# Kernel optimization log

Hardware: AMD Instinct MI355X
Metric: run time of the kernel (lower is better)

## Reference

```python
import jax, jax.numpy as jnp
import numpy as np

MC = 16384
IND_T = 96
N_MAT = 4
N_STRIKES = 21


def _init_linear(key, fan_in, fan_out, prefix=()):
    k1, k2 = jax.random.split(key)
    lim = 1.0 / np.sqrt(fan_in)
    W = jax.random.uniform(k1, prefix + (fan_in, fan_out), minval=-lim, maxval=lim, dtype=jnp.float32)
    b = jax.random.uniform(k2, prefix + (fan_out,), minval=-lim, maxval=lim, dtype=jnp.float32)
    return W, b


def setup_inputs() -> dict:
    key = jax.random.key(0)
    ks = jax.random.split(key, 14)
    z = jax.random.normal(ks[0], (MC, IND_T), dtype=jnp.float32)
    zz = jax.random.normal(ks[1], (MC, IND_T), dtype=jnp.float32)
    timegrid = jnp.arange(IND_T + 1, dtype=jnp.float32) / 365.0  # daily grid
    maturities = jnp.array([24, 48, 72, 96], dtype=jnp.int32)    # in days
    strikes = jnp.linspace(0.8, 1.2, N_STRIKES, dtype=jnp.float32)
    sv_W1, sv_b1 = _init_linear(ks[2], 3, 100)
    sv_W2, sv_b2 = _init_linear(ks[3], 100, 100)
    sv_W3, sv_b3 = _init_linear(ks[4], 100, 1)
    vh_W1, vh_b1 = _init_linear(ks[5], 2, 20, (N_MAT,))
    vh_W2, vh_b2 = _init_linear(ks[6], 20, N_STRIKES, (N_MAT,))
    vd_W1, vd_b1 = _init_linear(ks[7], 1, 20)
    vd_W2, vd_b2 = _init_linear(ks[8], 20, 1)
    vv_W1, vv_b1 = _init_linear(ks[9], 1, 20)
    vv_W2, vv_b2 = _init_linear(ks[10], 20, 1)
    v0 = jax.random.uniform(ks[11], (1,), dtype=jnp.float32) * 0.1
    rho = jnp.ones((1,), dtype=jnp.float32) * -2.0
    return dict(S0=jnp.float32(1.0), rate=jnp.float32(0.05), z=z, zz=zz,
                timegrid=timegrid, strikes=strikes, v0=v0, rho=rho,
                sv_W1=sv_W1, sv_b1=sv_b1, sv_W2=sv_W2, sv_b2=sv_b2, sv_W3=sv_W3, sv_b3=sv_b3,
                vh_W1=vh_W1, vh_b1=vh_b1, vh_W2=vh_W2, vh_b2=vh_b2,
                vd_W1=vd_W1, vd_b1=vd_b1, vd_W2=vd_W2, vd_b2=vd_b2,
                vv_W1=vv_W1, vv_b1=vv_b1, vv_W2=vv_W2, vv_b2=vv_b2,
                maturities=maturities)


def reference(S0, rate, z, zz, timegrid, strikes, v0, rho,
              sv_W1, sv_b1, sv_W2, sv_b2, sv_W3, sv_b3,
              vh_W1, vh_b1, vh_W2, vh_b2,
              vd_W1, vd_b1, vd_W2, vd_b2,
              vv_W1, vv_b1, vv_W2, vv_b2,
              maturities):
    sg = jax.lax.stop_gradient
    mc = z.shape[0]
    n_mat = vh_W1.shape[0]
    n_strikes = strikes.shape[0]

    def s_vol(x):  # [MC,3] -> [MC,1], softplus output
        h1 = jax.nn.relu(x @ sv_W1 + sv_b1)
        h2 = jax.nn.relu(h1 @ sv_W2 + sv_b2)
        return jax.nn.softplus(h2 @ sv_W3 + sv_b3)

    def v_drift(v):  # [MC,1] -> [MC,1]
        return jax.nn.relu(v @ vd_W1 + vd_b1) @ vd_W2 + vd_b2

    def v_vol(v):  # [MC,1] -> [MC,1], softplus output
        return jax.nn.softplus(jax.nn.relu(v @ vv_W1 + vv_b1) @ vv_W2 + vv_b2)

    def vanilla_hedge_all(x):  # [MC,2] -> [MC, n_strikes, n_mat] (one net per maturity)
        h1 = jax.nn.relu(jnp.einsum('mi,kio->kmo', x, vh_W1) + vh_b1[:, None, :])
        out = jax.nn.softplus(jnp.einsum('kmo,koj->kmj', h1, vh_W2) + vh_b2[:, None, :])
        return jnp.transpose(out, (1, 2, 0))

    rho_t = jnp.tanh(rho)[0]
    days = jnp.round(timegrid * 365.0).astype(jnp.int32)       # [IND_T+1]
    le = days[1:, None] <= maturities[None, :]                  # [IND_T, n_mat]
    idx_net = jnp.argmax(le, axis=1)                            # first live maturity per step
    is_mat = jnp.any(days[1:, None] == maturities[None, :], axis=1)
    mat_idx = jnp.arange(n_mat)

    Slog0 = jnp.log(jnp.full((mc, 1), S0, dtype=jnp.float32))
    V0 = jnp.full((mc, 1), 1.0, dtype=jnp.float32) * jax.nn.sigmoid(v0)[0] * 0.5
    cv0 = jnp.zeros((mc, n_strikes, n_mat), dtype=jnp.float32)
    pv0 = jnp.zeros((n_mat, n_strikes), dtype=jnp.float32)

    xs = (z.T[:, :, None], zz.T[:, :, None], timegrid[:-1], timegrid[1:], idx_net, is_mat)

    def step(carry, x):
        Slog_old, V_old, cv, pv_h, pv_var = carry
        z_i, zz_i, t0, t1, idx, im = x
        h = t1 - t0
        sqh = jnp.sqrt(h)
        dW = sqh * z_i                                          # [MC,1]
        dB = rho_t * dW + jnp.sqrt(1.0 - rho_t ** 2) * sqh * zz_i
        ones_t = jnp.full((mc, 1), 1.0, dtype=jnp.float32) * t0
        pd = s_vol(jnp.concatenate([ones_t, Slog_old, V_old], axis=1))  # price diffusion
        cv_fwd = vanilla_hedge_all(jnp.concatenate([ones_t, sg(Slog_old)], axis=1))
        V_new = V_old + v_drift(V_old) * h + v_vol(V_old) * dB
        drift = rate - 0.5 * pd ** 2
        diff = pd * dW
        drift_c = 1.0 + jnp.abs(sg(drift)) * sqh                # tamed Euler
        diff_c = 1.0 + jnp.abs(sg(pd)) * sqh
        Slog_new = Slog_old + drift * h / drift_c + diff / diff_c
        S_new = jnp.exp(Slog_new)
        S_old = jnp.exp(Slog_old)
        dS = jnp.exp(-rate * t1) * S_new - jnp.exp(-rate * t0) * S_old  # [MC,1]
        mask = (mat_idx >= idx).astype(cv.dtype)                # live maturities only
        cv = cv + mask[None, None, :] * cv_fwd * sg(dS)[:, :, None]
        # hedged vanilla (call) prices collected at maturity steps
        payoff = jnp.exp(-rate * t1) * jnp.maximum(S_new - strikes[None, :], 0.0)
        price = payoff - cv[:, :, idx]                          # [MC, n_strikes]
        pv = jnp.mean(price, axis=0)
        pvar = jnp.var(price, axis=0, ddof=1)
        sel = (mat_idx == idx)[:, None] & im
        pv_h = jnp.where(sel, pv[None, :], pv_h)
        pv_var = jnp.where(sel, pvar[None, :], pv_var)
        return (Slog_new, V_new, cv, pv_h, pv_var), None

    (_, _, _, pv_h, pv_var), _ = jax.lax.scan(step, (Slog0, V0, cv0, pv0, pv0), xs)
    return jnp.stack([pv_h, pv_var])  # [2, n_mat, n_strikes]
```

## Files before the change

kernel.cpp:

```cpp
#include <hip/hip_runtime.h>
#include <hip/hip_bf16.h>
#include <math.h>


#define MC      16384
#define NSTEP   96
#define BLOCK   1024
#define NGROUP  256
#define NPAIR   84

typedef short bf16x8 __attribute__((ext_vector_type(8)));
typedef float f32x4  __attribute__((ext_vector_type(4)));

union U8 { uint4 u; bf16x8 v; };
union BF2U { __hip_bfloat162 b; unsigned u; };

__device__ __forceinline__ unsigned bf16rne(float x) {
    unsigned u = __float_as_uint(x);
    return (u + 0x7FFFu + ((u >> 16) & 1u)) >> 16;
}
__device__ __forceinline__ unsigned pk2(float lo, float hi) {
    BF2U t; t.b = __float22bfloat162_rn(make_float2(lo, hi));
    return t.u;
}
__device__ __forceinline__ float sp(float x) {
    return fmaxf(x, 0.f) + __logf(1.f + __expf(-fabsf(x)));
}

__global__ __launch_bounds__(BLOCK, 4)
void lsv_sim(const float* __restrict__ S0p,   const float* __restrict__ ratep,
             const float* __restrict__ z,     const float* __restrict__ zzg,
             const float* __restrict__ strikesg,
             const float* __restrict__ v0p,   const float* __restrict__ rhop,
             const float* __restrict__ svW1,  const float* __restrict__ svb1,
             const float* __restrict__ svW2,  const float* __restrict__ svb2,
             const float* __restrict__ svW3,  const float* __restrict__ svb3,
             const float* __restrict__ vhW1,  const float* __restrict__ vhb1,
             const float* __restrict__ vhW2,  const float* __restrict__ vhb2,
             const float* __restrict__ vdW1,  const float* __restrict__ vdb1,
             const float* __restrict__ vdW2,  const float* __restrict__ vdb2,
             const float* __restrict__ vvW1,  const float* __restrict__ vvb1,
             const float* __restrict__ vvW2,  const float* __restrict__ vvb2,
             const int*   __restrict__ mats,
             float* __restrict__ psum, float* __restrict__ psq)
{
    __shared__ __align__(16) unsigned short H1c[16 * 64 * 8];
    __shared__ __align__(16) float W1f[16 * 32];
    __shared__ __align__(16) float WH1f[16 * 32];
    __shared__ __align__(16) float B2T[128], W3T[128];
    __shared__ float RED[64 * 4];
    __shared__ float VDl[2][64], VVl[2][64];
    __shared__ float PSs[4][32], PSq[4][32];
    __shared__ float VW[128];

    const int tid  = threadIdx.x;
    const int lane = tid & 63;
    const int w    = __builtin_amdgcn_readfirstlane(tid >> 6);
    const int quad = lane >> 4;
    const int col  = lane & 15;
    const int gpath = blockIdx.x * 64 + lane;

    const int pt = w & 3;
    const int jg = w >> 2;
    const int hm = w >> 2;

    for (int e = tid; e < 128; e += BLOCK) {
        float v = 0.f;
        if      (e < 20)             v = vdW1[e];
        else if (e < 40)             v = vdb1[e - 20];
        else if (e < 60)             v = vdW2[e - 40];
        else if (e >= 64 && e < 84)  v = vvW1[e - 64];
        else if (e >= 84 && e < 104) v = vvb1[e - 84];
        else if (e >= 104 && e < 124)v = vvW2[e - 104];
        else if (e == 124)           v = vdb2[0];
        else if (e == 125)           v = vvb2[0];
        VW[e] = v;
        B2T[e] = (e < 100) ? svb2[e] : 0.f;
        W3T[e] = (e < 100) ? svW3[e] : 0.f;
    }
    for (int e = tid; e < 512; e += BLOCK) {
        const int kc2 = e >> 5, r5 = e & 31, grp = r5 >> 3, kk = kc2 * 8 + (r5 & 7);
        float v = 0.f;
        if (kk < 100) v = (grp == 0) ? svW1[kk] : (grp == 1) ? svW1[100 + kk]
                        : (grp == 2) ? svW1[200 + kk] : svb1[kk];
        W1f[e] = v;
    }
    for (int e = tid; e < 512; e += BLOCK) {
        const int hq = e >> 5, r5 = e & 31, grp = r5 >> 3;
        const int hmm = hq >> 2, qq = hq & 3;
        const int j = qq * 8 + (r5 & 7);
        float v = 0.f;
        if (j < 20 && grp < 3)
            v = (grp == 0) ? vhW1[hmm * 40 + j] : (grp == 1) ? vhW1[hmm * 40 + 20 + j]
                                                : vhb1[hmm * 20 + j];
        WH1f[e] = v;
    }

    const float rate  = ratep[0];
    const float S0    = S0p[0];
    const float rho_t = tanhf(rhop[0]);
    const float srho  = sqrtf(1.f - rho_t * rho_t);
    const float b3    = svb3[0];
    int matr[4];
#pragma unroll
    for (int k = 0; k < 4; k++) matr[k] = mats[k];

    bf16x8 Af[4][2];
#pragma unroll
    for (int c = 0; c < 4; c++)
#pragma unroll
        for (int t = 0; t < 2; t++) {
            U8 tt;
#pragma unroll
            for (int e2 = 0; e2 < 4; e2++) {
                const int k0 = 32 * c + 8 * quad + 2 * e2;
                const int j  = (2 * jg + t) * 16 + col;
                const float v0 = (k0     < 100 && j < 100) ? svW2[k0 * 100 + j]       : 0.f;
                const float v1 = (k0 + 1 < 100 && j < 100) ? svW2[(k0 + 1) * 100 + j] : 0.f;
                (&tt.u.x)[e2] = bf16rne(v0) | (bf16rne(v1) << 16);
            }
            Af[c][t] = tt.v;
        }
    bf16x8 Ah[2];
#pragma unroll
    for (int st = 0; st < 2; st++) {
        U8 tt;
#pragma unroll
        for (int e2 = 0; e2 < 4; e2++) {
            const int j0 = 8 * quad + 2 * e2, j1 = j0 + 1;
            const int s  = st * 16 + col;
            const float v0 = (j0 < 20 && s < 21) ? vhW2[hm * 420 + j0 * 21 + s] : 0.f;
            const float v1 = (j1 < 20 && s < 21) ? vhW2[hm * 420 + j1 * 21 + s] : 0.f;
            (&tt.u.x)[e2] = bf16rne(v0) | (bf16rne(v1) << 16);
        }
        Ah[st] = tt.v;
    }
    float b2h0[4], b2h1[4], K0a[4], K1a[4];
#pragma unroll
    for (int r = 0; r < 4; r++) {
        const int s0 = quad * 4 + r, s1 = 16 + quad * 4 + r;
        b2h0[r] = vhb2[hm * 21 + s0];
        K0a[r]  = strikesg[s0];
        b2h1[r] = (s1 < 21) ? vhb2[hm * 21 + s1] : 0.f;
        K1a[r]  = (s1 < 21) ? strikesg[s1] : 1e30f;
    }

    float Slog = __logf(S0);
    float S    = __expf(Slog);
    float V    = (1.f / (1.f + __expf(-v0p[0]))) * 0.5f;
    f32x4 cv0 = {0.f, 0.f, 0.f, 0.f};
    f32x4 cv1 = {0.f, 0.f, 0.f, 0.f};
    float Slog_prev = 0.f, dS_prev = 0.f, disc1_prev = 1.f, t0_prev = 0.f;
    int   idx_prev = 0;
    bool  im_prev  = false;

    const float* zrow  = z   + (size_t)gpath * NSTEP;
    const float* zzrow = zzg + (size_t)gpath * NSTEP;

    const int path = pt * 16 + col;
    const int kc   = jg * 4 + quad;

    __syncthreads();

    auto hedge_step = [&]() {
        if (hm >= idx_prev) {
            const float slp = __shfl(Slog_prev, path);
            U8 b;
#pragma unroll
            for (int hh = 0; hh < 2; hh++) {
                const float* Wp = WH1f + (hm * 4 + quad) * 32 + hh * 4;
                const float4 wt4 = *reinterpret_cast<const float4*>(Wp);
                const float4 ws4 = *reinterpret_cast<const float4*>(Wp + 8);
                const float4 bb4 = *reinterpret_cast<const float4*>(Wp + 16);
                const float x0 = fmaxf(bb4.x + t0_prev * wt4.x + slp * ws4.x, 0.f);
                const float x1 = fmaxf(bb4.y + t0_prev * wt4.y + slp * ws4.y, 0.f);
                const float x2 = fmaxf(bb4.z + t0_prev * wt4.z + slp * ws4.z, 0.f);
                const float x3 = fmaxf(bb4.w + t0_prev * wt4.w + slp * ws4.w, 0.f);
                (&b.u.x)[2 * hh]     = pk2(x0, x1);
                (&b.u.x)[2 * hh + 1] = pk2(x2, x3);
            }
            const f32x4 z4 = {0.f, 0.f, 0.f, 0.f};
            const f32x4 D0 = __builtin_amdgcn_mfma_f32_16x16x32_bf16(Ah[0], b.v, z4, 0, 0, 0);
            const f32x4 D1 = __builtin_amdgcn_mfma_f32_16x16x32_bf16(Ah[1], b.v, z4, 0, 0, 0);
            const float dsP = __shfl(dS_prev, path);
#pragma unroll
            for (int r = 0; r < 4; r++) {
                cv0[r] += sp(D0[r] + b2h0[r]) * dsP;
                cv1[r] += sp(D1[r] + b2h1[r]) * dsP;
            }
            if (im_prev && hm == idx_prev) {
                const float Sp = __shfl(S, path);
                float p0[4], q0[4], p1[4], q1[4];
#pragma unroll
                for (int r = 0; r < 4; r++) {
                    p0[r] = disc1_prev * fmaxf(Sp - K0a[r], 0.f) - cv0[r];
                    p1[r] = disc1_prev * fmaxf(Sp - K1a[r], 0.f) - cv1[r];
                    q0[r] = p0[r] * p0[r];
                    q1[r] = p1[r] * p1[r];
                }
#pragma unroll
                for (int o = 1; o <= 8; o <<= 1) {
#pragma unroll
                    for (int r = 0; r < 4; r++) {
                        p0[r] += __shfl_xor(p0[r], o);
                        q0[r] += __shfl_xor(q0[r], o);
                        p1[r] += __shfl_xor(p1[r], o);
                        q1[r] += __shfl_xor(q1[r], o);
                    }
                }
                if (col == 0) {
#pragma unroll
                    for (int r = 0; r < 4; r++) {
                        const int s0 = quad * 4 + r, s1 = 16 + quad * 4 + r;
                        PSs[pt][s0] = p0[r];  PSq[pt][s0] = q0[r];
                        if (s1 < 21) { PSs[pt][s1] = p1[r];  PSq[pt][s1] = q1[r]; }
                    }
                }
            }
        }
    };

    auto ps_reduce = [&]() {
        if (w == 0 && im_prev) {
            const int s = lane & 31;
            if (s < 21) {
                const float* src = (lane >= 32) ? &PSq[0][0] : &PSs[0][0];
                const float acc = src[s] + src[32 + s] + src[64 + s] + src[96 + s];
                float* dst = (lane >= 32) ? psq : psum;
                dst[(idx_prev * 21 + s) * NGROUP + blockIdx.x] = acc;
            }
        }
    };

    for (int i = 0; i < NSTEP; i++) {
        const float zi  = zrow[i];
        const float zzi = zzrow[i];

        const float t0    = (float)i       * (1.f / 365.f);
        const float t1    = (float)(i + 1) * (1.f / 365.f);
        const float h     = t1 - t0;
        const float sqh   = sqrtf(h);
        const float disc0 = __expf(-rate * t0);
        const float disc1 = __expf(-rate * t1);
        const int   day   = i + 1;
        const int   idx   = (day > matr[0]) + (day > matr[1]) + (day > matr[2]);
        const bool  im    = (day == matr[idx]);

        {
            const float slp = __shfl(Slog, path);
            const float vp  = __shfl(V, path);
            const float* Wp = W1f + kc * 32;
            uint4 o;
#pragma unroll
            for (int hh = 0; hh < 2; hh++) {
                const float4 a4 = *reinterpret_cast<const float4*>(Wp + hh * 4);
                const float4 b4 = *reinterpret_cast<const float4*>(Wp + 8 + hh * 4);
                const float4 c4 = *reinterpret_cast<const float4*>(Wp + 16 + hh * 4);
                const float4 d4 = *reinterpret_cast<const float4*>(Wp + 24 + hh * 4);
                const float x0 = fmaxf(d4.x + t0 * a4.x + slp * b4.x + vp * c4.x, 0.f);
                const float x1 = fmaxf(d4.y + t0 * a4.y + slp * b4.y + vp * c4.y, 0.f);
                const float x2 = fmaxf(d4.z + t0 * a4.z + slp * b4.z + vp * c4.z, 0.f);
                const float x3 = fmaxf(d4.w + t0 * a4.w + slp * b4.w + vp * c4.w, 0.f);
                (&o.x)[2 * hh]     = pk2(x0, x1);
                (&o.x)[2 * hh + 1] = pk2(x2, x3);
            }
            *reinterpret_cast<uint4*>(H1c + (kc * 64 + path) * 8) = o;
        }
        if (i > 0) hedge_step();
        if (w == 14) {
            float a2 = 0.f;
#pragma unroll
            for (int q5 = 0; q5 < 5; q5++) {
                const float4 w1 = *reinterpret_cast<const float4*>(VW + 4 * q5);
                const float4 b1 = *reinterpret_cast<const float4*>(VW + 20 + 4 * q5);
                const float4 w2 = *reinterpret_cast<const float4*>(VW + 40 + 4 * q5);
                a2 += fmaxf(V * w1.x + b1.x, 0.f) * w2.x;
                a2 += fmaxf(V * w1.y + b1.y, 0.f) * w2.y;
                a2 += fmaxf(V * w1.z + b1.z, 0.f) * w2.z;
                a2 += fmaxf(V * w1.w + b1.w, 0.f) * w2.w;
            }
            VDl[i & 1][lane] = a2;
        }
        if (w == 15) {
            float a2 = 0.f;
#pragma unroll
            for (int q5 = 0; q5 < 5; q5++) {
                const float4 w1 = *reinterpret_cast<const float4*>(VW + 64 + 4 * q5);
                const float4 b1 = *reinterpret_cast<const float4*>(VW + 84 + 4 * q5);
                const float4 w2 = *reinterpret_cast<const float4*>(VW + 104 + 4 * q5);
                a2 += fmaxf(V * w1.x + b1.x, 0.f) * w2.x;
                a2 += fmaxf(V * w1.y + b1.y, 0.f) * w2.y;
                a2 += fmaxf(V * w1.z + b1.z, 0.f) * w2.z;
                a2 += fmaxf(V * w1.w + b1.w, 0.f) * w2.w;
            }
            VVl[i & 1][lane] = a2;
        }
        __syncthreads();

        {
            f32x4 d0 = {0.f, 0.f, 0.f, 0.f};
            f32x4 d1 = {0.f, 0.f, 0.f, 0.f};
#pragma unroll
            for (int c = 0; c < 4; c++) {
                const bf16x8 b = *reinterpret_cast<const bf16x8*>(
                    H1c + ((quad + 4 * c) * 64 + path) * 8);
                d0 = __builtin_amdgcn_mfma_f32_16x16x32_bf16(Af[c][0], b, d0, 0, 0, 0);
                d1 = __builtin_amdgcn_mfma_f32_16x16x32_bf16(Af[c][1], b, d1, 0, 0, 0);
            }
            const int j0 = (2 * jg) * 16 + quad * 4;
            const float4 b2a = *reinterpret_cast<const float4*>(B2T + j0);
            const float4 w3a = *reinterpret_cast<const float4*>(W3T + j0);
            const float4 b2b = *reinterpret_cast<const float4*>(B2T + j0 + 16);
            const float4 w3b = *reinterpret_cast<const float4*>(W3T + j0 + 16);
            float acc = fmaxf(d0[0] + b2a.x, 0.f) * w3a.x
                      + fmaxf(d0[1] + b2a.y, 0.f) * w3a.y
                      + fmaxf(d0[2] + b2a.z, 0.f) * w3a.z
                      + fmaxf(d0[3] + b2a.w, 0.f) * w3a.w
                      + fmaxf(d1[0] + b2b.x, 0.f) * w3b.x
                      + fmaxf(d1[1] + b2b.y, 0.f) * w3b.y
                      + fmaxf(d1[2] + b2b.z, 0.f) * w3b.z
                      + fmaxf(d1[3] + b2b.w, 0.f) * w3b.w;
            acc += __shfl_xor(acc, 16);
            acc += __shfl_xor(acc, 32);
            if (quad == 0)
                RED[path * 4 + jg] = acc;
        }
        ps_reduce();
        __syncthreads();

        {
            const float4 rr = *reinterpret_cast<const float4*>(RED + lane * 4);
            const float pout = (rr.x + rr.y) + (rr.z + rr.w);
            const float pd = sp(pout + b3);
            const float vdv = VDl[i & 1][lane] + VW[124];
            const float vvv = sp(VVl[i & 1][lane] + VW[125]);
            const float dW = sqh * zi;
            const float dB = rho_t * dW + srho * sqh * zzi;
            const float Vn = V + vdv * h + vvv * dB;
            const float drift   = rate - 0.5f * pd * pd;
            const float diff    = pd * dW;
            const float drift_c = 1.f + fabsf(drift) * sqh;
            const float diff_c  = 1.f + fabsf(pd) * sqh;
            const float Sln = Slog + __fdividef(drift * h, drift_c) + __fdividef(diff, diff_c);
            const float Sn  = __expf(Sln);
            const float dS  = disc1 * Sn - disc0 * S;
            Slog_prev = Slog; dS_prev = dS; disc1_prev = disc1; t0_prev = t0;
            idx_prev = idx; im_prev = im;
            Slog = Sln; S = Sn; V = Vn;
        }
    }

    hedge_step();
    __syncthreads();
    ps_reduce();
}

__global__ void lsv_finalize(const float* __restrict__ psum,
                             const float* __restrict__ psq,
                             float* __restrict__ out)
{
    const int t = blockIdx.x * blockDim.x + threadIdx.x;
    if (t >= NPAIR) return;
    float s = 0.f, q = 0.f;
    for (int b = 0; b < NGROUP; b++) {
        s += psum[t * NGROUP + b];
        q += psq [t * NGROUP + b];
    }
    const float mean = s * (1.0f / (float)MC);
    const float var  = (q - (float)MC * mean * mean) * (1.0f / (float)(MC - 1));
    out[t]         = mean;
    out[NPAIR + t] = var;
}

extern "C" void kernel_launch(void* const* d_in, const int* in_sizes, int n_in,
                              void* d_out, int out_size, void* d_ws, size_t ws_size,
                              hipStream_t stream)
{
    const float* S0    = (const float*)d_in[0];
    const float* rate  = (const float*)d_in[1];
    const float* z     = (const float*)d_in[2];
    const float* zz    = (const float*)d_in[3];
    const float* strikes = (const float*)d_in[5];
    const float* v0    = (const float*)d_in[6];
    const float* rho   = (const float*)d_in[7];
    const float* svW1  = (const float*)d_in[8];
    const float* svb1  = (const float*)d_in[9];
    const float* svW2  = (const float*)d_in[10];
    const float* svb2  = (const float*)d_in[11];
    const float* svW3  = (const float*)d_in[12];
    const float* svb3  = (const float*)d_in[13];
    const float* vhW1  = (const float*)d_in[14];
    const float* vhb1  = (const float*)d_in[15];
    const float* vhW2  = (const float*)d_in[16];
    const float* vhb2  = (const float*)d_in[17];
    const float* vdW1  = (const float*)d_in[18];
    const float* vdb1  = (const float*)d_in[19];
    const float* vdW2  = (const float*)d_in[20];
    const float* vdb2  = (const float*)d_in[21];
    const float* vvW1  = (const float*)d_in[22];
    const float* vvb1  = (const float*)d_in[23];
    const float* vvW2  = (const float*)d_in[24];
    const float* vvb2  = (const float*)d_in[25];
    const int*   mats  = (const int*)d_in[26];

    float* psum = (float*)d_ws;
    float* psq  = psum + NPAIR * NGROUP;

    hipLaunchKernelGGL(lsv_sim, dim3(NGROUP), dim3(BLOCK), 0, stream,
                       S0, rate, z, zz, strikes, v0, rho,
                       svW1, svb1, svW2, svb2, svW3, svb3,
                       vhW1, vhb1, vhW2, vhb2,
                       vdW1, vdb1, vdW2, vdb2,
                       vvW1, vvb1, vvW2, vvb2,
                       mats, psum, psq);

    hipLaunchKernelGGL(lsv_finalize, dim3(1), dim3(128), 0, stream,
                       psum, psq, (float*)d_out);
}
```

Before: 434.4 us.

## Halve paths per block to 32, remap waves, fuse finalize, precompute step table

Each block now simulates 32 paths with 512 threads (8 waves), and the grid grows to 512 blocks. The per-step MLP and hedge work is remapped so each wave owns one 16-column tile across two path groups. The H1 LDS layout gets an XOR swizzle and padded weight rows to reduce bank conflicts. Per-step time and discount constants are precomputed into a shared table, the vol/drift MLPs merge into one wave, and the finalize kernel is folded in through a last-block atomic counter, which adds a memset. The goal is more blocks in flight for better latency hiding and less per-step scalar work, with fewer waves per block sharing the MFMA load.

New measurement: 487.8 us. 12.3% more time.

```diff
diff --git a/kernel.cpp b/kernel.cpp
--- a/kernel.cpp
+++ b/kernel.cpp
@@ -5,8 +5,9 @@
 
 #define MC      16384
 #define NSTEP   96
-#define BLOCK   1024
-#define NGROUP  256
+#define NPATH   32
+#define BLOCK   512
+#define NGROUP  512
 #define NPAIR   84
 
 typedef short bf16x8 __attribute__((ext_vector_type(8)));
@@ -42,27 +43,30 @@
              const float* __restrict__ vvW1,  const float* __restrict__ vvb1,
              const float* __restrict__ vvW2,  const float* __restrict__ vvb2,
              const int*   __restrict__ mats,
-             float* __restrict__ psum, float* __restrict__ psq)
+             float* __restrict__ psum, float* __restrict__ psq,
+             unsigned* __restrict__ cnt, float* __restrict__ out)
 {
-    __shared__ __align__(16) unsigned short H1c[16 * 64 * 8];
-    __shared__ __align__(16) float W1f[16 * 32];
-    __shared__ __align__(16) float WH1f[16 * 32];
+    __shared__ __align__(16) unsigned short H1c[NPATH * 16 * 8];
+    __shared__ __align__(16) float W1f[16 * 36];
+    __shared__ __align__(16) float WH1f[16 * 36];
     __shared__ __align__(16) float B2T[128], W3T[128];
-    __shared__ float RED[64 * 4];
-    __shared__ float VDl[2][64], VVl[2][64];
-    __shared__ float PSs[4][32], PSq[4][32];
+    __shared__ __align__(16) float4 STa[96], STb[96];
+    __shared__ float RED[8][32];
+    __shared__ float VDl[2][32], VVl[2][32];
+    __shared__ float PSs[32], PSq[32];
     __shared__ float VW[128];
+    __shared__ unsigned lastv;
 
     const int tid  = threadIdx.x;
     const int lane = tid & 63;
     const int w    = __builtin_amdgcn_readfirstlane(tid >> 6);
     const int quad = lane >> 4;
     const int col  = lane & 15;
-    const int gpath = blockIdx.x * 64 + lane;
-
-    const int pt = w & 3;
-    const int jg = w >> 2;
-    const int hm = w >> 2;
+    const int pidx = lane & 31;
+    const int gpath = blockIdx.x * NPATH + pidx;
+
+    const int hm    = w >> 1;
+    const int stile = w & 1;
 
     for (int e = tid; e < 128; e += BLOCK) {
         float v = 0.f;
@@ -78,71 +82,82 @@
         B2T[e] = (e < 100) ? svb2[e] : 0.f;
         W3T[e] = (e < 100) ? svW3[e] : 0.f;
     }
-    for (int e = tid; e < 512; e += BLOCK) {
-        const int kc2 = e >> 5, r5 = e & 31, grp = r5 >> 3, kk = kc2 * 8 + (r5 & 7);
+    for (int e = tid; e < 576; e += BLOCK) {
+        const int kc2 = e / 36, r6 = e - 36 * kc2;
         float v = 0.f;
-        if (kk < 100) v = (grp == 0) ? svW1[kk] : (grp == 1) ? svW1[100 + kk]
-                        : (grp == 2) ? svW1[200 + kk] : svb1[kk];
+        if (r6 < 32) {
+            const int grp = r6 >> 3, kk = kc2 * 8 + (r6 & 7);
+            if (kk < 100) v = (grp == 0) ? svW1[kk] : (grp == 1) ? svW1[100 + kk]
+                            : (grp == 2) ? svW1[200 + kk] : svb1[kk];
+        }
         W1f[e] = v;
     }
-    for (int e = tid; e < 512; e += BLOCK) {
-        const int hq = e >> 5, r5 = e & 31, grp = r5 >> 3;
+    for (int e = tid; e < 576; e += BLOCK) {
+        const int hq = e / 36, r6 = e - 36 * hq;
         const int hmm = hq >> 2, qq = hq & 3;
-        const int j = qq * 8 + (r5 & 7);
         float v = 0.f;
-        if (j < 20 && grp < 3)
-            v = (grp == 0) ? vhW1[hmm * 40 + j] : (grp == 1) ? vhW1[hmm * 40 + 20 + j]
-                                                : vhb1[hmm * 20 + j];
+        if (r6 < 24) {
+            const int grp = r6 >> 3, j = qq * 8 + (r6 & 7);
+            if (j < 20)
+                v = (grp == 0) ? vhW1[hmm * 40 + j] : (grp == 1) ? vhW1[hmm * 40 + 20 + j]
+                                                    : vhb1[hmm * 20 + j];
+        }
         WH1f[e] = v;
     }
+    if (tid < 96) {
+        const int i = tid;
+        const float t0 = (float)i       * (1.f / 365.f);
+        const float t1 = (float)(i + 1) * (1.f / 365.f);
+        const float hh = t1 - t0;
+        const float rr = ratep[0];
+        const int  day = i + 1;
+        const int  mm0 = mats[0], mm1 = mats[1], mm2 = mats[2], mm3 = mats[3];
+        const int  idx = (day > mm0) + (day > mm1) + (day > mm2);
+        const int  mday = (idx == 0) ? mm0 : (idx == 1) ? mm1 : (idx == 2) ? mm2 : mm3;
+        STa[i] = make_float4(t0, hh, sqrtf(hh), __expf(-rr * t0));
+        STb[i] = make_float4(__expf(-rr * t1), (float)idx, (day == mday) ? 1.f : 0.f, 0.f);
+    }
+    if (tid < 32) RED[7][tid] = 0.f;
 
     const float rate  = ratep[0];
     const float S0    = S0p[0];
     const float rho_t = tanhf(rhop[0]);
     const float srho  = sqrtf(1.f - rho_t * rho_t);
     const float b3    = svb3[0];
-    int matr[4];
-#pragma unroll
-    for (int k = 0; k < 4; k++) matr[k] = mats[k];
-
-    bf16x8 Af[4][2];
-#pragma unroll
-    for (int c = 0; c < 4; c++)
-#pragma unroll
-        for (int t = 0; t < 2; t++) {
-            U8 tt;
-#pragma unroll
-            for (int e2 = 0; e2 < 4; e2++) {
-                const int k0 = 32 * c + 8 * quad + 2 * e2;
-                const int j  = (2 * jg + t) * 16 + col;
-                const float v0 = (k0     < 100 && j < 100) ? svW2[k0 * 100 + j]       : 0.f;
-                const float v1 = (k0 + 1 < 100 && j < 100) ? svW2[(k0 + 1) * 100 + j] : 0.f;
-                (&tt.u.x)[e2] = bf16rne(v0) | (bf16rne(v1) << 16);
-            }
-            Af[c][t] = tt.v;
-        }
-    bf16x8 Ah[2];
-#pragma unroll
-    for (int st = 0; st < 2; st++) {
+
+    bf16x8 Af[4];
+#pragma unroll
+    for (int c = 0; c < 4; c++) {
+        U8 tt;
+#pragma unroll
+        for (int e2 = 0; e2 < 4; e2++) {
+            const int k0 = 32 * c + 8 * quad + 2 * e2;
+            const int j  = w * 16 + col;
+            const float v0 = (k0     < 100 && j < 100) ? svW2[k0 * 100 + j]       : 0.f;
+            const float v1 = (k0 + 1 < 100 && j < 100) ? svW2[(k0 + 1) * 100 + j] : 0.f;
+            (&tt.u.x)[e2] = bf16rne(v0) | (bf16rne(v1) << 16);
+        }
+        Af[c] = tt.v;
+    }
+    bf16x8 Ah;
+    {
         U8 tt;
 #pragma unroll
         for (int e2 = 0; e2 < 4; e2++) {
             const int j0 = 8 * quad + 2 * e2, j1 = j0 + 1;
-            const int s  = st * 16 + col;
+            const int s  = stile * 16 + col;
             const float v0 = (j0 < 20 && s < 21) ? vhW2[hm * 420 + j0 * 21 + s] : 0.f;
             const float v1 = (j1 < 20 && s < 21) ? vhW2[hm * 420 + j1 * 21 + s] : 0.f;
             (&tt.u.x)[e2] = bf16rne(v0) | (bf16rne(v1) << 16);
         }
-        Ah[st] = tt.v;
-    }
-    float b2h0[4], b2h1[4], K0a[4], K1a[4];
+        Ah = tt.v;
+    }
+    float b2h[4], Ka[4];
 #pragma unroll
     for (int r = 0; r < 4; r++) {
-        const int s0 = quad * 4 + r, s1 = 16 + quad * 4 + r;
-        b2h0[r] = vhb2[hm * 21 + s0];
-        K0a[r]  = strikesg[s0];
-        b2h1[r] = (s1 < 21) ? vhb2[hm * 21 + s1] : 0.f;
-        K1a[r]  = (s1 < 21) ? strikesg[s1] : 1e30f;
+        const int s = stile * 16 + quad * 4 + r;
+        b2h[r] = (s < 21) ? vhb2[hm * 21 + s] : 0.f;
+        Ka[r]  = (s < 21) ? strikesg[s] : 1e30f;
     }
 
     float Slog = __logf(S0);
@@ -157,63 +172,65 @@
     const float* zrow  = z   + (size_t)gpath * NSTEP;
     const float* zzrow = zzg + (size_t)gpath * NSTEP;
 
-    const int path = pt * 16 + col;
-    const int kc   = jg * 4 + quad;
+    const int p1p = tid >> 4;
+    const int kc1 = tid & 15;
 
     __syncthreads();
 
     auto hedge_step = [&]() {
         if (hm >= idx_prev) {
-            const float slp = __shfl(Slog_prev, path);
-            U8 b;
+            const float slp0 = __shfl(Slog_prev, col);
+            const float slp1 = __shfl(Slog_prev, 16 + col);
+            const float* Wp = WH1f + (hm * 4 + quad) * 36;
+            U8 b0f, b1f;
 #pragma unroll
             for (int hh = 0; hh < 2; hh++) {
-                const float* Wp = WH1f + (hm * 4 + quad) * 32 + hh * 4;
-                const float4 wt4 = *reinterpret_cast<const float4*>(Wp);
-                const float4 ws4 = *reinterpret_cast<const float4*>(Wp + 8);
-                const float4 bb4 = *reinterpret_cast<const float4*>(Wp + 16);
-                const float x0 = fmaxf(bb4.x + t0_prev * wt4.x + slp * ws4.x, 0.f);
-                const float x1 = fmaxf(bb4.y + t0_prev * wt4.y + slp * ws4.y, 0.f);
-                const float x2 = fmaxf(bb4.z + t0_prev * wt4.z + slp * ws4.z, 0.f);
-                const float x3 = fmaxf(bb4.w + t0_prev * wt4.w + slp * ws4.w, 0.f);
-                (&b.u.x)[2 * hh]     = pk2(x0, x1);
-                (&b.u.x)[2 * hh + 1] = pk2(x2, x3);
+                const float4 wt4 = *reinterpret_cast<const float4*>(Wp + hh * 4);
+                const float4 ws4 = *reinterpret_cast<const float4*>(Wp + 8 + hh * 4);
+                const float4 bb4 = *reinterpret_cast<const float4*>(Wp + 16 + hh * 4);
+                const float c0 = bb4.x + t0_prev * wt4.x;
+                const float c1 = bb4.y + t0_prev * wt4.y;
+                const float c2 = bb4.z + t0_prev * wt4.z;
+                const float c3 = bb4.w + t0_prev * wt4.w;
+                (&b0f.u.x)[2 * hh]     = pk2(fmaxf(c0 + slp0 * ws4.x, 0.f), fmaxf(c1 + slp0 * ws4.y, 0.f));
+                (&b0f.u.x)[2 * hh + 1] = pk2(fmaxf(c2 + slp0 * ws4.z, 0.f), fmaxf(c3 + slp0 * ws4.w, 0.f));
+                (&b1f.u.x)[2 * hh]     = pk2(fmaxf(c0 + slp1 * ws4.x, 0.f), fmaxf(c1 + slp1 * ws4.y, 0.f));
+                (&b1f.u.x)[2 * hh + 1] = pk2(fmaxf(c2 + slp1 * ws4.z, 0.f), fmaxf(c3 + slp1 * ws4.w, 0.f));
             }
             const f32x4 z4 = {0.f, 0.f, 0.f, 0.f};
-            const f32x4 D0 = __builtin_amdgcn_mfma_f32_16x16x32_bf16(Ah[0], b.v, z4, 0, 0, 0);
-            const f32x4 D1 = __builtin_amdgcn_mfma_f32_16x16x32_bf16(Ah[1], b.v, z4, 0, 0, 0);
-            const float dsP = __shfl(dS_prev, path);
+            const f32x4 D0 = __builtin_amdgcn_mfma_f32_16x16x32_bf16(Ah, b0f.v, z4, 0, 0, 0);
+            const f32x4 D1 = __builtin_amdgcn_mfma_f32_16x16x32_bf16(Ah, b1f.v, z4, 0, 0, 0);
+            const float ds0 = __shfl(dS_prev, col);
+            const float ds1 = __shfl(dS_prev, 16 + col);
 #pragma unroll
             for (int r = 0; r < 4; r++) {
-                cv0[r] += sp(D0[r] + b2h0[r]) * dsP;
-                cv1[r] += sp(D1[r] + b2h1[r]) * dsP;
+                cv0[r] += sp(D0[r] + b2h[r]) * ds0;
+                cv1[r] += sp(D1[r] + b2h[r]) * ds1;
             }
             if (im_prev && hm == idx_prev) {
-                const float Sp = __shfl(S, path);
-                float p0[4], q0[4], p1[4], q1[4];
+                const float Sp0 = __shfl(S, col);
+                const float Sp1 = __shfl(S, 16 + col);
+                float st[4], sq[4];
 #pragma unroll
                 for (int r = 0; r < 4; r++) {
-                    p0[r] = disc1_prev * fmaxf(Sp - K0a[r], 0.f) - cv0[r];
-                    p1[r] = disc1_prev * fmaxf(Sp - K1a[r], 0.f) - cv1[r];
-                    q0[r] = p0[r] * p0[r];
-                    q1[r] = p1[r] * p1[r];
+                    const float p0 = disc1_prev * fmaxf(Sp0 - Ka[r], 0.f) - cv0[r];
+                    const float p1 = disc1_prev * fmaxf(Sp1 - Ka[r], 0.f) - cv1[r];
+                    st[r] = p0 + p1;
+                    sq[r] = p0 * p0 + p1 * p1;
                 }
 #pragma unroll
                 for (int o = 1; o <= 8; o <<= 1) {
 #pragma unroll
                     for (int r = 0; r < 4; r++) {
-                        p0[r] += __shfl_xor(p0[r], o);
-                        q0[r] += __shfl_xor(q0[r], o);
-                        p1[r] += __shfl_xor(p1[r], o);
-                        q1[r] += __shfl_xor(q1[r], o);
+                        st[r] += __shfl_xor(st[r], o);
+                        sq[r] += __shfl_xor(sq[r], o);
                     }
                 }
                 if (col == 0) {
 #pragma unroll
                     for (int r = 0; r < 4; r++) {
-                        const int s0 = quad * 4 + r, s1 = 16 + quad * 4 + r;
-                        PSs[pt][s0] = p0[r];  PSq[pt][s0] = q0[r];
-                        if (s1 < 21) { PSs[pt][s1] = p1[r];  PSq[pt][s1] = q1[r]; }
+                        const int s = stile * 16 + quad * 4 + r;
+                        if (s < 21) { PSs[s] = st[r]; PSq[s] = sq[r]; }
                     }
                 }
             }
@@ -224,10 +241,9 @@
         if (w == 0 && im_prev) {
             const int s = lane & 31;
             if (s < 21) {
-                const float* src = (lane >= 32) ? &PSq[0][0] : &PSs[0][0];
-                const float acc = src[s] + src[32 + s] + src[64 + s] + src[96 + s];
+                const float val = (lane >= 32) ? PSq[s] : PSs[s];
                 float* dst = (lane >= 32) ? psq : psum;
-                dst[(idx_prev * 21 + s) * NGROUP + blockIdx.x] = acc;
+                dst[(idx_prev * 21 + s) * NGROUP + blockIdx.x] = val;
             }
         }
     };
@@ -235,21 +251,17 @@
     for (int i = 0; i < NSTEP; i++) {
         const float zi  = zrow[i];
         const float zzi = zzrow[i];
-
-        const float t0    = (float)i       * (1.f / 365.f);
-        const float t1    = (float)(i + 1) * (1.f / 365.f);
-        const float h     = t1 - t0;
-        const float sqh   = sqrtf(h);
-        const float disc0 = __expf(-rate * t0);
-        const float disc1 = __expf(-rate * t1);
-        const int   day   = i + 1;
-        const int   idx   = (day > matr[0]) + (day > matr[1]) + (day > matr[2]);
-        const bool  im    = (day == matr[idx]);
+        const float4 sa = STa[i];
+        const float4 sb = STb[i];
+        const float t0 = sa.x, h = sa.y, sqh = sa.z, disc0 = sa.w;
+        const float disc1 = sb.x;
+        const int   idx   = (int)sb.y;
+        const bool  im    = (sb.z != 0.f);
 
         {
-            const float slp = __shfl(Slog, path);
-            const float vp  = __shfl(V, path);
-            const float* Wp = W1f + kc * 32;
+            const float slp = __shfl(Slog, p1p);
+            const float vp  = __shfl(V, p1p);
+            const float* Wp = W1f + kc1 * 36;
             uint4 o;
 #pragma unroll
             for (int hh = 0; hh < 2; hh++) {
@@ -264,76 +276,67 @@
                 (&o.x)[2 * hh]     = pk2(x0, x1);
                 (&o.x)[2 * hh + 1] = pk2(x2, x3);
             }
-            *reinterpret_cast<uint4*>(H1c + (kc * 64 + path) * 8) = o;
+            const int slot = kc1 ^ (p1p & 15);
+            *reinterpret_cast<uint4*>(H1c + (p1p * 16 + slot) * 8) = o;
         }
         if (i > 0) hedge_step();
-        if (w == 14) {
+        if (w == 7) {
+            const float* Wb = VW + ((lane >> 5) << 6);
             float a2 = 0.f;
 #pragma unroll
             for (int q5 = 0; q5 < 5; q5++) {
-                const float4 w1 = *reinterpret_cast<const float4*>(VW + 4 * q5);
-                const float4 b1 = *reinterpret_cast<const float4*>(VW + 20 + 4 * q5);
-                const float4 w2 = *reinterpret_cast<const float4*>(VW + 40 + 4 * q5);
+                const float4 w1 = *reinterpret_cast<const float4*>(Wb + 4 * q5);
+                const float4 b1 = *reinterpret_cast<const float4*>(Wb + 20 + 4 * q5);
+                const float4 w2 = *reinterpret_cast<const float4*>(Wb + 40 + 4 * q5);
                 a2 += fmaxf(V * w1.x + b1.x, 0.f) * w2.x;
                 a2 += fmaxf(V * w1.y + b1.y, 0.f) * w2.y;
                 a2 += fmaxf(V * w1.z + b1.z, 0.f) * w2.z;
                 a2 += fmaxf(V * w1.w + b1.w, 0.f) * w2.w;
             }
-            VDl[i & 1][lane] = a2;
-        }
-        if (w == 15) {
-            float a2 = 0.f;
-#pragma unroll
-            for (int q5 = 0; q5 < 5; q5++) {
-                const float4 w1 = *reinterpret_cast<const float4*>(VW + 64 + 4 * q5);
-                const float4 b1 = *reinterpret_cast<const float4*>(VW + 84 + 4 * q5);
-                const float4 w2 = *reinterpret_cast<const float4*>(VW + 104 + 4 * q5);
-                a2 += fmaxf(V * w1.x + b1.x, 0.f) * w2.x;
-                a2 += fmaxf(V * w1.y + b1.y, 0.f) * w2.y;
-                a2 += fmaxf(V * w1.z + b1.z, 0.f) * w2.z;
-                a2 += fmaxf(V * w1.w + b1.w, 0.f) * w2.w;
-            }
-            VVl[i & 1][lane] = a2;
+            if (lane < 32) VDl[i & 1][pidx] = a2;
+            else           VVl[i & 1][pidx] = a2;
         }
         __syncthreads();
 
-        {
+        if (w < 7) {
             f32x4 d0 = {0.f, 0.f, 0.f, 0.f};
             f32x4 d1 = {0.f, 0.f, 0.f, 0.f};
+            const int rb0 = col * 16, rb1 = (16 + col) * 16;
 #pragma unroll
             for (int c = 0; c < 4; c++) {
-                const bf16x8 b = *reinterpret_cast<const bf16x8*>(
-                    H1c + ((quad + 4 * c) * 64 + path) * 8);
-                d0 = __builtin_amdgcn_mfma_f32_16x16x32_bf16(Af[c][0], b, d0, 0, 0, 0);
-                d1 = __builtin_amdgcn_mfma_f32_16x16x32_bf16(Af[c][1], b, d1, 0, 0, 0);
-            }
-            const int j0 = (2 * jg) * 16 + quad * 4;
+                const int slot = (4 * c + quad) ^ col;
+                const bf16x8 b0 = *reinterpret_cast<const bf16x8*>(H1c + (rb0 + slot) * 8);
+                const bf16x8 b1 = *reinterpret_cast<const bf16x8*>(H1c + (rb1 + slot) * 8);
+                d0 = __builtin_amdgcn_mfma_f32_16x16x32_bf16(Af[c], b0, d0, 0, 0, 0);
+                d1 = __builtin_amdgcn_mfma_f32_16x16x32_bf16(Af[c], b1, d1, 0, 0, 0);
+            }
+            const int j0 = w * 16 + quad * 4;
             const float4 b2a = *reinterpret_cast<const float4*>(B2T + j0);
             const float4 w3a = *reinterpret_cast<const float4*>(W3T + j0);
-            const float4 b2b = *reinterpret_cast<const float4*>(B2T + j0 + 16);
-            const float4 w3b = *reinterpret_cast<const float4*>(W3T + j0 + 16);
-            float acc = fmaxf(d0[0] + b2a.x, 0.f) * w3a.x
-                      + fmaxf(d0[1] + b2a.y, 0.f) * w3a.y
-                      + fmaxf(d0[2] + b2a.z, 0.f) * w3a.z
-                      + fmaxf(d0[3] + b2a.w, 0.f) * w3a.w
-                      + fmaxf(d1[0] + b2b.x, 0.f) * w3b.x
-                      + fmaxf(d1[1] + b2b.y, 0.f) * w3b.y
-                      + fmaxf(d1[2] + b2b.z, 0.f) * w3b.z
-                      + fmaxf(d1[3] + b2b.w, 0.f) * w3b.w;
-            acc += __shfl_xor(acc, 16);
-            acc += __shfl_xor(acc, 32);
-            if (quad == 0)
-                RED[path * 4 + jg] = acc;
+            float acc0 = fmaxf(d0[0] + b2a.x, 0.f) * w3a.x
+                       + fmaxf(d0[1] + b2a.y, 0.f) * w3a.y
+                       + fmaxf(d0[2] + b2a.z, 0.f) * w3a.z
+                       + fmaxf(d0[3] + b2a.w, 0.f) * w3a.w;
+            float acc1 = fmaxf(d1[0] + b2a.x, 0.f) * w3a.x
+                       + fmaxf(d1[1] + b2a.y, 0.f) * w3a.y
+                       + fmaxf(d1[2] + b2a.z, 0.f) * w3a.z
+                       + fmaxf(d1[3] + b2a.w, 0.f) * w3a.w;
+            acc0 += __shfl_xor(acc0, 16);  acc0 += __shfl_xor(acc0, 32);
+            acc1 += __shfl_xor(acc1, 16);  acc1 += __shfl_xor(acc1, 32);
+            if (quad == 0) {
+                RED[w][col]      = acc0;
+                RED[w][16 + col] = acc1;
+            }
         }
         ps_reduce();
         __syncthreads();
 
         {
-            const float4 rr = *reinterpret_cast<const float4*>(RED + lane * 4);
-            const float pout = (rr.x + rr.y) + (rr.z + rr.w);
+            float pout = RED[0][pidx] + RED[1][pidx] + RED[2][pidx] + RED[3][pidx]
+                       + RED[4][pidx] + RED[5][pidx] + RED[6][pidx] + RED[7][pidx];
             const float pd = sp(pout + b3);
-            const float vdv = VDl[i & 1][lane] + VW[124];
-            const float vvv = sp(VVl[i & 1][lane] + VW[125]);
+            const float vdv = VDl[i & 1][pidx] + VW[124];
+            const float vvv = sp(VVl[i & 1][pidx] + VW[125]);
             const float dW = sqh * zi;
             const float dB = rho_t * dW + srho * sqh * zzi;
             const float Vn = V + vdv * h + vvv * dB;
@@ -353,23 +356,31 @@
     hedge_step();
     __syncthreads();
     ps_reduce();
-}
-
-__global__ void lsv_finalize(const float* __restrict__ psum,
-                             const float* __restrict__ psq,
-                             float* __restrict__ out)
-{
-    const int t = blockIdx.x * blockDim.x + threadIdx.x;
-    if (t >= NPAIR) return;
-    float s = 0.f, q = 0.f;
-    for (int b = 0; b < NGROUP; b++) {
-        s += psum[t * NGROUP + b];
-        q += psq [t * NGROUP + b];
-    }
-    const float mean = s * (1.0f / (float)MC);
-    const float var  = (q - (float)MC * mean * mean) * (1.0f / (float)(MC - 1));
-    out[t]         = mean;
-    out[NPAIR + t] = var;
+
+    __threadfence();
+    __syncthreads();
+    if (tid == 0) lastv = atomicAdd(cnt, 1u);
+    __syncthreads();
+    if (lastv == NGROUP - 1) {
+        __threadfence();
+        const int t   = tid >> 2;
+        const int sub = tid & 3;
+        if (t < NPAIR) {
+            const float* ps = psum + t * NGROUP + sub * 128;
+            const float* pq = psq  + t * NGROUP + sub * 128;
+            float s = 0.f, q = 0.f;
+#pragma unroll 4
+            for (int b = 0; b < 128; b++) { s += ps[b]; q += pq[b]; }
+            s += __shfl_xor(s, 1);  s += __shfl_xor(s, 2);
+            q += __shfl_xor(q, 1);  q += __shfl_xor(q, 2);
+            if (sub == 0) {
+                const float mean = s * (1.0f / (float)MC);
+                const float var  = (q - (float)MC * mean * mean) * (1.0f / (float)(MC - 1));
+                out[t]         = mean;
+                out[NPAIR + t] = var;
+            }
+        }
+    }
 }
 
 extern "C" void kernel_launch(void* const* d_in, const int* in_sizes, int n_in,
@@ -403,8 +414,11 @@
     const float* vvb2  = (const float*)d_in[25];
     const int*   mats  = (const int*)d_in[26];
 
-    float* psum = (float*)d_ws;
-    float* psq  = psum + NPAIR * NGROUP;
+    float*    psum = (float*)d_ws;
+    float*    psq  = psum + NPAIR * NGROUP;
+    unsigned* cnt  = (unsigned*)(psq + NPAIR * NGROUP);
+
+    hipMemsetAsync((void*)cnt, 0, sizeof(unsigned), stream);
 
     hipLaunchKernelGGL(lsv_sim, dim3(NGROUP), dim3(BLOCK), 0, stream,
                        S0, rate, z, zz, strikes, v0, rho,
@@ -412,8 +426,5 @@
                        vhW1, vhb1, vhW2, vhb2,
                        vdW1, vdb1, vdW2, vdb2,
                        vvW1, vvb1, vvW2, vvb2,
-                       mats, psum, psq);
-
-    hipLaunchKernelGGL(lsv_finalize, dim3(1), dim3(128), 0, stream,
-                       psum, psq, (float*)d_out);
+                       mats, psum, psq, cnt, (float*)d_out);
 }
```
